# Kernel tuning notes

Measured on AMD Instinct MI355X. Metric: run time of the kernel, lower is better.

## Reference

```python
import jax, jax.numpy as jnp
import numpy as np

# Hard-coded constants from the original module
GAMMA = 0.1      # self.gamma default
N_STEPS = 10     # self.n_steps default
RHO = 0.9        # RMSProp decay
LR = 0.009       # RMSProp learning rate
MOM = 0.9        # momentum
EPS = 1e-8       # RMSProp epsilon
ABS_EPS = 1e-6   # diff_abs smoothing: diff_abs(x) = sqrt(x^2 + 1e-6)

B, IN_DIM, OUT_DIM = 4096, 2048, 4096


def setup_inputs() -> dict:
    key = jax.random.key(0)
    k1, k2 = jax.random.split(key)
    inputs = jax.random.normal(k1, (B, IN_DIM), dtype=jnp.float32)
    # keras 'uniform' init: U(-0.05, 0.05), shape (output_dim, input_dim)
    W = jax.random.uniform(k2, (OUT_DIM, IN_DIM), minval=-0.05, maxval=0.05, dtype=jnp.float32)
    return {"inputs": inputs, "W": W}


def reference(inputs, W):
    batch = inputs.shape[0]
    out_dim = W.shape[0]
    a = jnp.sqrt(inputs * inputs + ABS_EPS)          # diff_abs(inputs), [B, in_dim]
    act = lambda u: 0.5 * (1.0 + jnp.exp(-u))        # self.activation

    def cost(x):
        # l1_norm.sum() + l1_inov + own_norm  (prior = 0)
        l1 = (GAMMA * act(x @ W) * a).sum()
        l1_inov = (GAMMA / 10.0) * jnp.sum(x * x)
        own = GAMMA * jnp.sum(jnp.sqrt(x * x + ABS_EPS))
        return l1 + l1_inov + own

    grad_cost = jax.grad(cost)

    def step(carry, _):
        x, acc1, acc2 = carry
        g = grad_cost(x)                              # [B, out_dim]
        new_acc1 = RHO * acc1 + (1.0 - RHO) * g * g
        denom = jnp.sqrt(new_acc1 + EPS)
        new_acc2 = MOM * acc2 - LR * g / denom
        cand = x - LR * g / denom
        t = 0.1 * LR / denom                          # elementwise prox threshold
        new_x = jnp.maximum(cand - t, 0.0) + jnp.minimum(cand + t, 0.0) + MOM * new_acc2
        new_x = jax.lax.stop_gradient(new_x)          # theano disconnected_grad
        return (new_x, new_acc1, new_acc2), None

    z = jnp.zeros((batch, out_dim), dtype=inputs.dtype)
    # scan runs n_steps; last step's l1_norm uses the state after n_steps-1 updates,
    # so run n_steps-1 updates then compute the final l1_norm directly.
    (x, _, _), _ = jax.lax.scan(step, (z, z, z), None, length=N_STEPS - 1)
    return GAMMA * act(x @ W) * a                     # outputs[-1][-1]: last l1_norm, [B, in_dim]
```

## Files before the change

### kernel.cpp

```cpp
#include <hip/hip_runtime.h>
#include <cstdint>
#include <cstddef>

#define B_DIM   4096
#define IN_DIM  2048
#define OUT_DIM 4096

typedef __attribute__((ext_vector_type(8))) __bf16 bf16x8;
typedef __attribute__((ext_vector_type(4))) float  f32x4;
typedef unsigned short ushortT;

__device__ __forceinline__ ushortT f2bf(float f) {
    unsigned int u = __float_as_uint(f);
    u += 0x7FFFu + ((u >> 16) & 1u);
    return (ushortT)(u >> 16);
}
__device__ __forceinline__ float bf2f(ushortT b) {
    return __uint_as_float(((unsigned int)b) << 16);
}

__device__ __forceinline__ void gload16(const void* g, void* l) {
    __builtin_amdgcn_global_load_lds(
        (const __attribute__((address_space(1))) void*)g,
        (__attribute__((address_space(3))) void*)l, 16, 0, 0);
}

__global__ void prep_g0_kernel(const float* __restrict__ in, ushortT* __restrict__ Gb) {
    int i = blockIdx.x * 256 + threadIdx.x;
    float4 v = reinterpret_cast<const float4*>(in)[i];
    ushort4 g;
    g.x = f2bf(-0.05f * sqrtf(v.x * v.x + 1e-6f));
    g.y = f2bf(-0.05f * sqrtf(v.y * v.y + 1e-6f));
    g.z = f2bf(-0.05f * sqrtf(v.z * v.z + 1e-6f));
    g.w = f2bf(-0.05f * sqrtf(v.w * v.w + 1e-6f));
    reinterpret_cast<ushort4*>(Gb)[i] = g;
}

__global__ void conv_w_kernel(const float* __restrict__ W, ushortT* __restrict__ Wb,
                              ushortT* __restrict__ WTb) {
    __shared__ float tile[64][65];
    const int i0 = blockIdx.x * 64;
    const int j0 = blockIdx.y * 64;
    const int c  = threadIdx.x & 63;
    const int rq = threadIdx.x >> 6;
#pragma unroll
    for (int rp = 0; rp < 16; ++rp) {
        int row = rp * 4 + rq;
        float w = W[(size_t)(j0 + row) * IN_DIM + i0 + c];
        tile[row][c] = w;
        Wb[(size_t)(j0 + row) * IN_DIM + i0 + c] = f2bf(w);
    }
    __syncthreads();
#pragma unroll
    for (int rp = 0; rp < 16; ++rp) {
        int row = rp * 4 + rq;
        WTb[(size_t)(i0 + row) * OUT_DIM + j0 + c] = f2bf(tile[c][row]);
    }
}

template <int EPI, int BM>
__global__ __launch_bounds__(512, 1)
void gemm_phase(const ushortT* __restrict__ A, const ushortT* __restrict__ Bm,
                int N, int K,
                const float* __restrict__ inb, ushortT* __restrict__ Gb,
                float* __restrict__ out,
                ushortT* __restrict__ acc1, ushortT* __restrict__ acc2,
                ushortT* __restrict__ xb) {
    constexpr int BN   = 256;
    constexpr int ASZ  = BM * 64;
    constexpr int BSZ  = BN * 64;
    constexpr int SLOT = ASZ + BSZ;
    constexpr int LA   = BM / 128;
    constexpr int LB   = BN / 128;
    constexpr int L    = LA + LB;
    constexpr int MR   = BM / 32;
    constexpr int HP   = MR / 2;
    __shared__ alignas(16) char smem[4 * SLOT];

    const int tid  = threadIdx.x;
    const int lane = tid & 63;
    const int w    = tid >> 6;
    const int wm   = w >> 2;
    const int wn   = w & 3;
    const int nbx  = N / BN;
    const int nwg  = gridDim.x;
    const int cpx  = nwg >> 3;
    const int bid  = (int)blockIdx.x;
    const int swz  = (bid & 7) * cpx + (bid >> 3);
    const int bx   = swz % nbx;
    const int by   = swz / nbx;
    const int row0 = by * BM;
    const int col0 = bx * BN;

    const size_t strideK2 = (size_t)K * 2;

    const char* gp[L]; int lo[L];
#pragma unroll
    for (int i = 0; i < LA; ++i) {
        int Lp  = i * 512 + tid;
        int row = Lp >> 2, sl = Lp & 3;
        int src = sl ^ ((row >> 1) & 3);
        gp[i] = (const char*)A + (size_t)(row0 + row) * strideK2 + src * 16;
        lo[i] = i * 8192 + w * 1024;
    }
#pragma unroll
    for (int i = 0; i < LB; ++i) {
        int Lp  = i * 512 + tid;
        int row = Lp >> 2, sl = Lp & 3;
        int src = sl ^ ((row >> 1) & 3);
        gp[LA + i] = (const char*)Bm + (size_t)(col0 + row) * strideK2 + src * 16;
        lo[LA + i] = ASZ + i * 8192 + w * 1024;
    }
    auto stage_all = [&](int tt) {
        char* sb = smem + (tt & 3) * SLOT;
        const size_t kb = (size_t)tt * 64;
#pragma unroll
        for (int c = 0; c < L; ++c) gload16(gp[c] + kb, sb + lo[c]);
    };
    auto stage_chunk = [&](int tt, int c) {
        gload16(gp[c] + (size_t)tt * 64, smem + (tt & 3) * SLOT + lo[c]);
    };

    int aRd[MR], bRd[4];
#pragma unroll
    for (int m = 0; m < MR; ++m) {
        int row = wm * (BM / 2) + m * 16 + (lane & 15);
        aRd[m] = row * 64 + (((lane >> 4) ^ ((row >> 1) & 3)) * 16);
    }
#pragma unroll
    for (int n = 0; n < 4; ++n) {
        int row = wn * 64 + n * 16 + (lane & 15);
        bRd[n] = ASZ + row * 64 + (((lane >> 4) ^ ((row >> 1) & 3)) * 16);
    }

    f32x4 acc[MR][4] = {};
    const int nt = K >> 5;

    stage_all(0); stage_all(1); stage_all(2);

    for (int tt = 0; tt < nt; tt += 2) {
        if (tt + 2 < nt) asm volatile("s_waitcnt vmcnt(%0)" :: "n"(L) : "memory");
        else             asm volatile("s_waitcnt vmcnt(0)"  ::: "memory");
        __builtin_amdgcn_s_barrier();
        __builtin_amdgcn_sched_barrier(0);

        bf16x8 bF[4];
#pragma unroll
        for (int p = 0; p < MR; ++p) {
            constexpr int C0 = 1, C1 = 1;
            const int sslot = p / HP;
            const int mp    = p % HP;
            const char* sb  = smem + ((tt + sslot) & 3) * SLOT;
            if (mp == 0) {
#pragma unroll
                for (int n = 0; n < 4; ++n)
                    bF[n] = *reinterpret_cast<const bf16x8*>(sb + bRd[n]);
            }
            bf16x8 aF0 = *reinterpret_cast<const bf16x8*>(sb + aRd[2 * mp]);
            bf16x8 aF1 = *reinterpret_cast<const bf16x8*>(sb + aRd[2 * mp + 1]);
#pragma unroll
            for (int c = p * 2 * L / MR; c < (p + 1) * 2 * L / MR; ++c) {
                const int tile = (c < L) ? (tt + 3) : (tt + 4);
                const int cc   = (c < L) ? c : c - L;
                if (tile < nt) stage_chunk(tile, cc);
            }
            asm volatile("s_waitcnt lgkmcnt(0)" ::: "memory");
            __builtin_amdgcn_sched_barrier(0);
            __builtin_amdgcn_s_setprio(1);
#pragma unroll
            for (int n = 0; n < 4; ++n)
                acc[2 * mp][n] = __builtin_amdgcn_mfma_f32_16x16x32_bf16(aF0, bF[n], acc[2 * mp][n], 0, 0, 0);
#pragma unroll
            for (int n = 0; n < 4; ++n)
                acc[2 * mp + 1][n] = __builtin_amdgcn_mfma_f32_16x16x32_bf16(aF1, bF[n], acc[2 * mp + 1][n], 0, 0, 0);
            __builtin_amdgcn_s_setprio(0);
            __builtin_amdgcn_s_barrier();
            __builtin_amdgcn_sched_barrier(0);
        }
    }

    __builtin_amdgcn_s_barrier();

    float* lep = (float*)(smem + w * 4352);
    const int li = lane >> 4;
    const int lc = lane & 15;
    const int row0w = row0 + wm * (BM / 2);
    const int col0w = col0 + wn * 64;
#pragma unroll
    for (int m = 0; m < MR; ++m) {
#pragma unroll
        for (int n = 0; n < 4; ++n)
#pragma unroll
            for (int i = 0; i < 4; ++i)
                lep[(li * 4 + i) * 68 + n * 16 + lc] = acc[m][n][i];
        asm volatile("s_waitcnt lgkmcnt(0)" ::: "memory");
        __builtin_amdgcn_sched_barrier(0);
#pragma unroll
        for (int rr = 0; rr < 4; ++rr) {
            const int row = rr + li * 4;
            float4 v = *reinterpret_cast<const float4*>(&lep[row * 68 + lc * 4]);
            const size_t idx  = (size_t)(row0w + m * 16 + row) * N + col0w + lc * 4;
            const size_t idx4 = idx >> 2;
            if constexpr (EPI == 0) {
                float4 iv = reinterpret_cast<const float4*>(inb)[idx4];
                ushort4 g;
                g.x = f2bf(-0.05f * sqrtf(iv.x * iv.x + 1e-6f) * expf(-v.x));
                g.y = f2bf(-0.05f * sqrtf(iv.y * iv.y + 1e-6f) * expf(-v.y));
                g.z = f2bf(-0.05f * sqrtf(iv.z * iv.z + 1e-6f) * expf(-v.z));
                g.w = f2bf(-0.05f * sqrtf(iv.w * iv.w + 1e-6f) * expf(-v.w));
                *reinterpret_cast<ushort4*>(&Gb[idx]) = g;
            } else if constexpr (EPI == 1) {
                float4 iv = reinterpret_cast<const float4*>(inb)[idx4];
                float4 o;
                o.x = 0.05f * (1.0f + expf(-v.x)) * sqrtf(iv.x * iv.x + 1e-6f);
                o.y = 0.05f * (1.0f + expf(-v.y)) * sqrtf(iv.y * iv.y + 1e-6f);
                o.z = 0.05f * (1.0f + expf(-v.z)) * sqrtf(iv.z * iv.z + 1e-6f);
                o.w = 0.05f * (1.0f + expf(-v.w)) * sqrtf(iv.w * iv.w + 1e-6f);
                reinterpret_cast<float4*>(out)[idx4] = o;
            } else {
                ushort4 xu  = *reinterpret_cast<const ushort4*>(&xb[idx]);
                ushort4 a1u = *reinterpret_cast<const ushort4*>(&acc1[idx]);
                ushort4 a2u = *reinterpret_cast<const ushort4*>(&acc2[idx]);
                float xs[4] = {bf2f(xu.x), bf2f(xu.y), bf2f(xu.z), bf2f(xu.w)};
                float vs[4] = {v.x, v.y, v.z, v.w};
                ushortT a1s[4] = {a1u.x, a1u.y, a1u.z, a1u.w};
                ushortT a2s[4] = {a2u.x, a2u.y, a2u.z, a2u.w};
                ushortT a1n[4], a2n[4], xbn[4];
#pragma unroll
                for (int j = 0; j < 4; ++j) {
                    float g    = vs[j] + 0.02f * xs[j] + 0.1f * xs[j] * rsqrtf(xs[j] * xs[j] + 1e-6f);
                    float a1   = 0.9f * bf2f(a1s[j]) + 0.1f * g * g;
                    float inv  = rsqrtf(a1 + 1e-8f);
                    float r_   = 0.009f * g * inv;
                    float a2   = 0.9f * bf2f(a2s[j]) - r_;
                    float cand = xs[j] - r_;
                    float t_   = 0.0009f * inv;
                    float xn   = fmaxf(cand - t_, 0.0f) + fminf(cand + t_, 0.0f) + 0.9f * a2;
                    a1n[j] = f2bf(a1); a2n[j] = f2bf(a2); xbn[j] = f2bf(xn);
                }
                *reinterpret_cast<ushort4*>(&acc1[idx]) = make_ushort4(a1n[0], a1n[1], a1n[2], a1n[3]);
                *reinterpret_cast<ushort4*>(&acc2[idx]) = make_ushort4(a2n[0], a2n[1], a2n[2], a2n[3]);
                *reinterpret_cast<ushort4*>(&xb[idx])   = make_ushort4(xbn[0], xbn[1], xbn[2], xbn[3]);
            }
        }
        asm volatile("s_waitcnt lgkmcnt(0)" ::: "memory");
    }
}

extern "C" void kernel_launch(void* const* d_in, const int* in_sizes, int n_in,
                              void* d_out, int out_size, void* d_ws, size_t ws_size,
                              hipStream_t stream) {
    const float* in = (const float*)d_in[0];
    const float* W  = (const float*)d_in[1];
    float* out = (float*)d_out;
    char* ws = (char*)d_ws;

    ushortT* acc1 = (ushortT*)(ws);
    ushortT* acc2 = (ushortT*)(ws + ((size_t)32  << 20));
    ushortT* xb   = (ushortT*)(ws + ((size_t)64  << 20));
    ushortT* Wb   = (ushortT*)(ws + ((size_t)96  << 20));
    ushortT* WTb  = (ushortT*)(ws + ((size_t)112 << 20));
    ushortT* Gb   = (ushortT*)(ws + ((size_t)128 << 20));

    hipMemsetAsync(ws, 0, (size_t)96 << 20, stream);

    prep_g0_kernel<<<dim3(B_DIM * IN_DIM / 4 / 256), dim3(256), 0, stream>>>(in, Gb);
    conv_w_kernel<<<dim3(IN_DIM / 64, OUT_DIM / 64), dim3(256), 0, stream>>>(W, Wb, WTb);

    for (int step = 0; step < 9; ++step) {
        if (step > 0) {
            gemm_phase<0, 128><<<dim3(256), dim3(512), 0, stream>>>(
                xb, WTb, IN_DIM, OUT_DIM, in, Gb, nullptr, nullptr, nullptr, nullptr);
        }
        gemm_phase<2, 256><<<dim3(256), dim3(512), 0, stream>>>(
            Gb, Wb, OUT_DIM, IN_DIM, nullptr, nullptr, nullptr, acc1, acc2, xb);
    }
    gemm_phase<1, 128><<<dim3(256), dim3(512), 0, stream>>>(
        xb, WTb, IN_DIM, OUT_DIM, in, nullptr, out, nullptr, nullptr, nullptr);
}
```

Before: 1.560 ms.

## Replace single-block GEMM with smaller multi-block tiles and simpler 3-stage pipeline

Replaces the one-workgroup-per-CU GEMM, which used 256-column tiles and a 4-slot LDS ring with interleaved chunk prefetch, by a templated kernel. The new kernel uses 128-column tiles, a 3-slot LDS ring, whole-tile prefetch two steps ahead and launch bounds that allow several workgroups per CU. Grids double to 512 blocks and each wave computes a fixed 64x64 sub-tile. The aim is more latency hiding through occupancy and a shorter, simpler main loop. In exchange, each tile reuses less data, and the removal of the per-phase barriers and fine-grained staging could expose load latency.

```diff
diff --git a/kernel.cpp b/kernel.cpp
--- a/kernel.cpp
+++ b/kernel.cpp
@@ -58,30 +58,29 @@
     }
 }
 
-template <int EPI, int BM>
-__global__ __launch_bounds__(512, 1)
-void gemm_phase(const ushortT* __restrict__ A, const ushortT* __restrict__ Bm,
-                int N, int K,
-                const float* __restrict__ inb, ushortT* __restrict__ Gb,
-                float* __restrict__ out,
-                ushortT* __restrict__ acc1, ushortT* __restrict__ acc2,
-                ushortT* __restrict__ xb) {
-    constexpr int BN   = 256;
-    constexpr int ASZ  = BM * 64;
-    constexpr int BSZ  = BN * 64;
-    constexpr int SLOT = ASZ + BSZ;
-    constexpr int LA   = BM / 128;
-    constexpr int LB   = BN / 128;
-    constexpr int L    = LA + LB;
-    constexpr int MR   = BM / 32;
-    constexpr int HP   = MR / 2;
-    __shared__ alignas(16) char smem[4 * SLOT];
+template <int EPI, int BM, int BN, int NT, int WMS>
+__global__ __launch_bounds__(NT, 4)
+void gemm_mb(const ushortT* __restrict__ A, const ushortT* __restrict__ Bm,
+             int N, int K,
+             const float* __restrict__ inb, ushortT* __restrict__ Gb,
+             float* __restrict__ out,
+             ushortT* __restrict__ acc1, ushortT* __restrict__ acc2,
+             ushortT* __restrict__ xb) {
+    constexpr int WAVES = NT / 64;
+    constexpr int WNS   = WAVES / WMS;
+    constexpr int ASZ   = BM * 64;
+    constexpr int BSZ   = BN * 64;
+    constexpr int SLOT  = ASZ + BSZ;
+    constexpr int CA    = (4 * BM) / NT;
+    constexpr int CB    = (4 * BN) / NT;
+    constexpr int L     = CA + CB;
+    __shared__ alignas(16) char smem[3 * SLOT];
 
     const int tid  = threadIdx.x;
     const int lane = tid & 63;
     const int w    = tid >> 6;
-    const int wm   = w >> 2;
-    const int wn   = w & 3;
+    const int wm   = w / WNS;
+    const int wn   = w % WNS;
     const int nbx  = N / BN;
     const int nwg  = gridDim.x;
     const int cpx  = nwg >> 3;
@@ -96,35 +95,32 @@
 
     const char* gp[L]; int lo[L];
 #pragma unroll
-    for (int i = 0; i < LA; ++i) {
-        int Lp  = i * 512 + tid;
+    for (int c = 0; c < CA; ++c) {
+        int Lp  = c * NT + tid;
         int row = Lp >> 2, sl = Lp & 3;
         int src = sl ^ ((row >> 1) & 3);
-        gp[i] = (const char*)A + (size_t)(row0 + row) * strideK2 + src * 16;
-        lo[i] = i * 8192 + w * 1024;
-    }
-#pragma unroll
-    for (int i = 0; i < LB; ++i) {
-        int Lp  = i * 512 + tid;
+        gp[c] = (const char*)A + (size_t)(row0 + row) * strideK2 + src * 16;
+        lo[c] = c * NT * 16 + w * 1024;
+    }
+#pragma unroll
+    for (int c = 0; c < CB; ++c) {
+        int Lp  = c * NT + tid;
         int row = Lp >> 2, sl = Lp & 3;
         int src = sl ^ ((row >> 1) & 3);
-        gp[LA + i] = (const char*)Bm + (size_t)(col0 + row) * strideK2 + src * 16;
-        lo[LA + i] = ASZ + i * 8192 + w * 1024;
-    }
-    auto stage_all = [&](int tt) {
-        char* sb = smem + (tt & 3) * SLOT;
+        gp[CA + c] = (const char*)Bm + (size_t)(col0 + row) * strideK2 + src * 16;
+        lo[CA + c] = ASZ + c * NT * 16 + w * 1024;
+    }
+    auto stage = [&](int tt) {
+        char* sb = smem + (tt % 3) * SLOT;
         const size_t kb = (size_t)tt * 64;
 #pragma unroll
         for (int c = 0; c < L; ++c) gload16(gp[c] + kb, sb + lo[c]);
     };
-    auto stage_chunk = [&](int tt, int c) {
-        gload16(gp[c] + (size_t)tt * 64, smem + (tt & 3) * SLOT + lo[c]);
-    };
-
-    int aRd[MR], bRd[4];
-#pragma unroll
-    for (int m = 0; m < MR; ++m) {
-        int row = wm * (BM / 2) + m * 16 + (lane & 15);
+
+    int aRd[4], bRd[4];
+#pragma unroll
+    for (int m = 0; m < 4; ++m) {
+        int row = wm * 64 + m * 16 + (lane & 15);
         aRd[m] = row * 64 + (((lane >> 4) ^ ((row >> 1) & 3)) * 16);
     }
 #pragma unroll
@@ -133,50 +129,31 @@
         bRd[n] = ASZ + row * 64 + (((lane >> 4) ^ ((row >> 1) & 3)) * 16);
     }
 
-    f32x4 acc[MR][4] = {};
+    f32x4 acc[4][4] = {};
     const int nt = K >> 5;
 
-    stage_all(0); stage_all(1); stage_all(2);
-
-    for (int tt = 0; tt < nt; tt += 2) {
-        if (tt + 2 < nt) asm volatile("s_waitcnt vmcnt(%0)" :: "n"(L) : "memory");
+    stage(0); stage(1);
+
+    for (int tt = 0; tt < nt; ++tt) {
+        if (tt < nt - 1) asm volatile("s_waitcnt vmcnt(%0)" :: "n"(L) : "memory");
         else             asm volatile("s_waitcnt vmcnt(0)"  ::: "memory");
         __builtin_amdgcn_s_barrier();
         __builtin_amdgcn_sched_barrier(0);
 
-        bf16x8 bF[4];
-#pragma unroll
-        for (int p = 0; p < MR; ++p) {
-            constexpr int C0 = 1, C1 = 1;
-            const int sslot = p / HP;
-            const int mp    = p % HP;
-            const char* sb  = smem + ((tt + sslot) & 3) * SLOT;
-            if (mp == 0) {
-#pragma unroll
-                for (int n = 0; n < 4; ++n)
-                    bF[n] = *reinterpret_cast<const bf16x8*>(sb + bRd[n]);
-            }
-            bf16x8 aF0 = *reinterpret_cast<const bf16x8*>(sb + aRd[2 * mp]);
-            bf16x8 aF1 = *reinterpret_cast<const bf16x8*>(sb + aRd[2 * mp + 1]);
-#pragma unroll
-            for (int c = p * 2 * L / MR; c < (p + 1) * 2 * L / MR; ++c) {
-                const int tile = (c < L) ? (tt + 3) : (tt + 4);
-                const int cc   = (c < L) ? c : c - L;
-                if (tile < nt) stage_chunk(tile, cc);
-            }
-            asm volatile("s_waitcnt lgkmcnt(0)" ::: "memory");
-            __builtin_amdgcn_sched_barrier(0);
-            __builtin_amdgcn_s_setprio(1);
+        const char* sb = smem + (tt % 3) * SLOT;
+        bf16x8 aF[4], bF[4];
+#pragma unroll
+        for (int n = 0; n < 4; ++n) bF[n] = *reinterpret_cast<const bf16x8*>(sb + bRd[n]);
+#pragma unroll
+        for (int m = 0; m < 4; ++m) aF[m] = *reinterpret_cast<const bf16x8*>(sb + aRd[m]);
+        if (tt + 2 < nt) stage(tt + 2);
+        __builtin_amdgcn_s_setprio(1);
+#pragma unroll
+        for (int m = 0; m < 4; ++m)
 #pragma unroll
             for (int n = 0; n < 4; ++n)
-                acc[2 * mp][n] = __builtin_amdgcn_mfma_f32_16x16x32_bf16(aF0, bF[n], acc[2 * mp][n], 0, 0, 0);
-#pragma unroll
-            for (int n = 0; n < 4; ++n)
-                acc[2 * mp + 1][n] = __builtin_amdgcn_mfma_f32_16x16x32_bf16(aF1, bF[n], acc[2 * mp + 1][n], 0, 0, 0);
-            __builtin_amdgcn_s_setprio(0);
-            __builtin_amdgcn_s_barrier();
-            __builtin_amdgcn_sched_barrier(0);
-        }
+                acc[m][n] = __builtin_amdgcn_mfma_f32_16x16x32_bf16(aF[m], bF[n], acc[m][n], 0, 0, 0);
+        __builtin_amdgcn_s_setprio(0);
     }
 
     __builtin_amdgcn_s_barrier();
@@ -184,10 +161,10 @@
     float* lep = (float*)(smem + w * 4352);
     const int li = lane >> 4;
     const int lc = lane & 15;
-    const int row0w = row0 + wm * (BM / 2);
+    const int row0w = row0 + wm * 64;
     const int col0w = col0 + wn * 64;
 #pragma unroll
-    for (int m = 0; m < MR; ++m) {
+    for (int m = 0; m < 4; ++m) {
 #pragma unroll
         for (int n = 0; n < 4; ++n)
 #pragma unroll
@@ -269,12 +246,12 @@
 
     for (int step = 0; step < 9; ++step) {
         if (step > 0) {
-            gemm_phase<0, 128><<<dim3(256), dim3(512), 0, stream>>>(
+            gemm_mb<0, 128, 128, 256, 2><<<dim3(512), dim3(256), 0, stream>>>(
                 xb, WTb, IN_DIM, OUT_DIM, in, Gb, nullptr, nullptr, nullptr, nullptr);
         }
-        gemm_phase<2, 256><<<dim3(256), dim3(512), 0, stream>>>(
+        gemm_mb<2, 256, 128, 512, 4><<<dim3(512), dim3(512), 0, stream>>>(
             Gb, Wb, OUT_DIM, IN_DIM, nullptr, nullptr, nullptr, acc1, acc2, xb);
     }
-    gemm_phase<1, 128><<<dim3(256), dim3(512), 0, stream>>>(
+    gemm_mb<1, 128, 128, 256, 2><<<dim3(512), dim3(256), 0, stream>>>(
         xb, WTb, IN_DIM, OUT_DIM, in, nullptr, out, nullptr, nullptr, nullptr);
 }
```

After: 1.663 ms. +6.6%, slower.
